# Performance work log

Measured on AMD Instinct MI355X. Metric: run time of the kernel, lower is better.

The kernel has to match this reference:

```python
import jax, jax.numpy as jnp
import numpy as np

B, H, W, C = 8, 32, 32, 384
NH, HD = 6, 64
SCALE = HD ** -0.5


def setup_inputs() -> dict:
    key = jax.random.key(0)
    ks = jax.random.split(key, 7)
    return {
        "x": jax.random.normal(ks[0], (B, H, W, C), jnp.float32),
        "qkv_w": jax.random.normal(ks[1], (C, 3 * C), jnp.float32) * 0.02,
        "qkv_b": jax.random.normal(ks[2], (3 * C,), jnp.float32) * 0.02,
        "proj_w": jax.random.normal(ks[3], (C, C), jnp.float32) * 0.02,
        "proj_b": jax.random.normal(ks[4], (C,), jnp.float32) * 0.02,
        "rel_pos_h": jax.random.normal(ks[5], (2 * H - 1, HD), jnp.float32) * 0.02,
        "rel_pos_w": jax.random.normal(ks[6], (2 * W - 1, HD), jnp.float32) * 0.02,
    }


def _get_rel_pos(rel_pos, q_size, k_size):
    # q_size == k_size and rel_pos already has 2*size-1 rows -> interpolation is identity
    coords = jnp.arange(q_size)[:, None] - jnp.arange(k_size)[None, :] + (k_size - 1)
    return rel_pos[coords]  # [q, k, head_dim]


def reference(x, qkv_w, qkv_b, proj_w, proj_b, rel_pos_h, rel_pos_w):
    b, h, w, c = x.shape
    hw = h * w
    qkv = x.reshape(b, hw, c) @ qkv_w + qkv_b            # [B, HW, 3C]
    qkv = qkv.reshape(b, hw, 3, NH, HD).transpose(2, 0, 3, 1, 4)
    qkv = qkv.reshape(3, b * NH, hw, HD)
    q, k, v = qkv[0], qkv[1], qkv[2]                      # [B*nH, HW, hd]

    attn = jnp.einsum('bqd,bkd->bqk', q * SCALE, k)       # [B*nH, HW, HW]

    Rh = _get_rel_pos(rel_pos_h, h, h)                    # [H, H, hd]
    Rw = _get_rel_pos(rel_pos_w, w, w)                    # [W, W, hd]
    r_q = q.reshape(b * NH, h, w, HD)
    rel_h = jnp.einsum('bhwc,hkc->bhwk', r_q, Rh)         # [B*nH, H, W, kH]
    rel_w = jnp.einsum('bhwc,wkc->bhwk', r_q, Rw)         # [B*nH, H, W, kW]
    attn = attn.reshape(b * NH, h, w, h, w) + rel_h[:, :, :, :, None] + rel_w[:, :, :, None, :]
    attn = attn.reshape(b * NH, hw, hw)

    attn = jax.nn.softmax(attn, axis=-1)
    out = jnp.einsum('bqk,bkd->bqd', attn, v)             # [B*nH, HW, hd]
    out = out.reshape(b, NH, h, w, HD).transpose(0, 2, 3, 1, 4).reshape(b, h, w, c)
    return out @ proj_w + proj_b
```

## Files before the change

kernel.cpp:

```cpp
#include <hip/hip_runtime.h>

typedef __attribute__((ext_vector_type(8))) short bf16x8;
typedef __attribute__((ext_vector_type(4))) float f32x4;

#define MFMA(a, b, c) __builtin_amdgcn_mfma_f32_16x16x32_bf16((a), (b), (c), 0, 0, 0)
#define LOG2E 1.4426950408889634f

__device__ __forceinline__ unsigned short f2bf(float f) {
    union { float f; unsigned u; } v; v.f = f;
    unsigned r = v.u + 0x7FFFu + ((v.u >> 16) & 1u);
    return (unsigned short)(r >> 16);
}
__device__ __forceinline__ float bf2f(unsigned short h) {
    union { unsigned u; float f; } v; v.u = ((unsigned)h) << 16;
    return v.f;
}
__device__ __forceinline__ float exp2fast(float x) {
#if __has_builtin(__builtin_amdgcn_exp2f)
    return __builtin_amdgcn_exp2f(x);
#else
    float r; asm("v_exp_f32 %0, %1" : "=v"(r) : "v"(x)); return r;
#endif
}
__device__ __forceinline__ void gload16(const void* g, void* l) {
    __builtin_amdgcn_global_load_lds(
        (const __attribute__((address_space(1))) void*)g,
        (__attribute__((address_space(3))) void*)l, 16, 0, 0);
}

#define WS_QHI   0
#define WS_QLO   6291456
#define WS_KHI   12582912
#define WS_KLO   18874368
#define WS_VTHI  25165824
#define WS_RELH  37748736
#define WS_RELW  40894464
#define WS_WTH   44040192
#define WS_WTL   44924928
#define WS_PWTH  45809664
#define WS_PWTL  46104576
#define WS_XHI   46399488
#define WS_XLO   52690944

__global__ __launch_bounds__(256) void prep_fused(const float* __restrict__ x,
        const float* __restrict__ qkv_w, const float* __restrict__ proj_w,
        unsigned short* __restrict__ xh,
        unsigned short* __restrict__ wth, unsigned short* __restrict__ pwth) {
    __shared__ float tile[64][65];
    const int bid = blockIdx.x;
    const int t = threadIdx.x;
    if (bid < 3072) {
        int i = bid * 256 + t;
        float4 v = ((const float4*)x)[i];
        float f[4] = {v.x, v.y, v.z, v.w};
#pragma unroll
        for (int j = 0; j < 4; ++j)
            xh[i * 4 + j] = f2bf(f[j]);
        return;
    }
    const float* w; unsigned short *oh; int K, N, bx, by;
    if (bid < 3180) {
        int b2 = bid - 3072;
        w = qkv_w; oh = wth; K = 384; N = 1152;
        bx = b2 % 18; by = b2 / 18;
    } else {
        int b3 = bid - 3180;
        w = proj_w; oh = pwth; K = 384; N = 384;
        bx = b3 % 6; by = b3 / 6;
    }
    const int k0 = by * 64, n0 = bx * 64;
#pragma unroll
    for (int i = 0; i < 16; ++i) {
        int idx = t + i * 256;
        int r = idx >> 6, c = idx & 63;
        tile[r][c] = w[(size_t)(k0 + r) * N + n0 + c];
    }
    __syncthreads();
#pragma unroll
    for (int i = 0; i < 16; ++i) {
        int idx = t + i * 256;
        int r = idx >> 6, c = idx & 63;
        oh[(size_t)(n0 + r) * K + k0 + c] = f2bf(tile[c][r]);
    }
}

__global__ __launch_bounds__(256) void qkv_gemm_mfma(
        const unsigned short* __restrict__ xh,
        const unsigned short* __restrict__ wth,
        const float* __restrict__ bias,
        unsigned short* __restrict__ qh,
        unsigned short* __restrict__ kh,
        unsigned short* __restrict__ vth) {
    __shared__ unsigned short Ah[2][4096], Bh[2][4096];
    const int t = threadIdx.x;
    const int lane = t & 63, wid = t >> 6;
    const int C = lane & 15, G = lane >> 4;
    const int nbid = (blockIdx.x & 7) * 288 + (blockIdx.x >> 3);
    const int row0 = (nbid / 18) * 64, col0 = (nbid % 18) * 64;
    const int rl = wid * 16 + (lane >> 3);
    const int cbyt = ((lane & 7) << 4) ^ ((lane >> 3) << 4);
    const char* pAh = (const char*)xh + (size_t)(row0 + rl) * 768 + cbyt;
    const char* pBh = (const char*)wth + (size_t)(col0 + rl) * 768 + cbyt;
    const int dof = wid * 2048;
    gload16(pAh, (char*)Ah[0] + dof); gload16(pAh + 6144, (char*)Ah[0] + dof + 1024);
    gload16(pBh, (char*)Bh[0] + dof); gload16(pBh + 6144, (char*)Bh[0] + dof + 1024);
    int cur = 0;
    f32x4 acc[4] = {};
    for (int kb = 0; kb < 6; ++kb) {
        if (kb < 5) {
            const int o = (kb + 1) * 128;
            gload16(pAh + o, (char*)Ah[cur^1] + dof); gload16(pAh + o + 6144, (char*)Ah[cur^1] + dof + 1024);
            gload16(pBh + o, (char*)Bh[cur^1] + dof); gload16(pBh + o + 6144, (char*)Bh[cur^1] + dof + 1024);
            __builtin_amdgcn_sched_barrier(0);
            asm volatile("s_waitcnt vmcnt(4)" ::: "memory");
        } else {
            asm volatile("s_waitcnt vmcnt(0)" ::: "memory");
        }
        __builtin_amdgcn_s_barrier();
        __builtin_amdgcn_sched_barrier(0);
        const unsigned short* AhB = Ah[cur];
        const unsigned short* BhB = Bh[cur];
#pragma unroll
        for (int ks = 0; ks < 2; ++ks) {
            int arow = wid * 16 + C;
            int aoff = arow * 128 + ((ks * 64 + G * 16) ^ ((arow & 7) << 4));
            bf16x8 ah = *(const bf16x8*)((char*)AhB + aoff);
#pragma unroll
            for (int s = 0; s < 4; ++s) {
                int brow = s * 16 + C;
                int boff = brow * 128 + ((ks * 64 + G * 16) ^ ((brow & 7) << 4));
                bf16x8 bh = *(const bf16x8*)((char*)BhB + boff);
                acc[s] = MFMA(ah, bh, acc[s]);
            }
        }
        __builtin_amdgcn_s_barrier();
        cur ^= 1;
    }
#pragma unroll
    for (int s = 0; s < 4; ++s) {
        int n = col0 + s * 16 + C;
        float bv = bias[n];
        int tsel = n / 384;
        int rem = n - tsel * 384;
        int head = rem >> 6, d = rem & 63;
#pragma unroll
        for (int r = 0; r < 4; ++r) {
            int m = row0 + wid * 16 + 4 * G + r;
            int b = m >> 10, hw = m & 1023;
            int g = b * 6 + head;
            float val = acc[s][r] + bv;
            if (tsel == 0) val *= 0.125f * LOG2E;
            unsigned short h = f2bf(val);
            if (tsel == 2) {
                vth[((size_t)g * 64 + d) * 1024 + hw] = h;
            } else {
                size_t o = ((size_t)g * 1024 + hw) * 64 + d;
                if (tsel == 0) qh[o] = h;
                else           kh[o] = h;
            }
        }
    }
}

__global__ __launch_bounds__(256) void rel_mfma(
        const unsigned short* __restrict__ qh,
        const float* __restrict__ rph, const float* __restrict__ rpw,
        unsigned short* __restrict__ relh, unsigned short* __restrict__ relw) {
    __shared__ unsigned short Bs[32 * 64];
    const int t = threadIdx.x;
    const int lane = t & 63, wid = t >> 6;
    const int C = lane & 15, G = lane >> 4;
    const int pos = blockIdx.x;
    const int g0 = blockIdx.y * 8;
    const int mode = blockIdx.z;
    const float* rp = (mode == 0) ? rph : rpw;
    {
        int k = t >> 3, d8 = t & 7;
        const float* src = rp + (size_t)(pos + 31 - k) * 64 + d8 * 8;
        float4 f0 = *(const float4*)src;
        float4 f1 = *(const float4*)(src + 4);
        unsigned short hv[8] = { f2bf(f0.x), f2bf(f0.y), f2bf(f0.z), f2bf(f0.w),
                                 f2bf(f1.x), f2bf(f1.y), f2bf(f1.z), f2bf(f1.w) };
        int bo = k * 128 + ((d8 * 16) ^ ((k & 7) << 4));
        *(bf16x8*)((char*)Bs + bo) = *(bf16x8*)hv;
    }
    __syncthreads();
    bf16x8 bf[2][2];
#pragma unroll
    for (int s = 0; s < 2; ++s)
#pragma unroll
        for (int ks = 0; ks < 2; ++ks) {
            int row = s * 16 + C;
            int off = row * 128 + ((ks * 64 + G * 16) ^ ((row & 7) << 4));
            bf[s][ks] = *(const bf16x8*)((char*)Bs + off);
        }
#pragma unroll
    for (int ib = 0; ib < 4; ++ib) {
        int arow = ib * 64 + wid * 16 + C;
        int gi = arow >> 5, w = arow & 31;
        int hw = (mode == 0) ? (pos * 32 + w) : (w * 32 + pos);
        const unsigned short* qrow = qh + ((size_t)(g0 + gi) * 1024 + hw) * 64;
        bf16x8 a0 = *(const bf16x8*)(qrow + G * 8);
        bf16x8 a1 = *(const bf16x8*)(qrow + 32 + G * 8);
        f32x4 acc[2] = {};
#pragma unroll
        for (int s = 0; s < 2; ++s) {
            acc[s] = MFMA(a0, bf[s][0], acc[s]);
            acc[s] = MFMA(a1, bf[s][1], acc[s]);
        }
        unsigned short* dst = (mode == 0) ? relh : relw;
#pragma unroll
        for (int s = 0; s < 2; ++s)
#pragma unroll
            for (int rr = 0; rr < 4; ++rr) {
                int orow = ib * 64 + wid * 16 + 4 * G + rr;
                int ogi = orow >> 5, ow = orow & 31;
                int ohw = (mode == 0) ? (pos * 32 + ow) : (ow * 32 + pos);
                dst[((size_t)(g0 + ogi) * 1024 + ohw) * 32 + s * 16 + C] =
                    f2bf(acc[s][rr] * 8.0f);
            }
    }
}

__global__ __launch_bounds__(256) void attn_mfma(
        const unsigned short* __restrict__ qh,
        const unsigned short* __restrict__ kh_g,
        const unsigned short* __restrict__ vth_g,
        const unsigned short* __restrict__ relh, const unsigned short* __restrict__ relw,
        unsigned short* __restrict__ atth) {
    __shared__ unsigned short Kh[2][4096], Vh[2][4096];
    __shared__ unsigned short Pl[4][1024];
    __shared__ unsigned short RelU[4][16 * 34];
    const int t = threadIdx.x;
    const int lane = t & 63, wid = t >> 6;
    const int C = lane & 15, G = lane >> 4;
    const int bid = blockIdx.x;
    const int wgid = (bid & 7) * 96 + (bid >> 3);
    const int g = wgid >> 4, qb = wgid & 15;
    const int qtile = qb * 64 + wid * 16;

    {
        const unsigned short* src = relh + ((size_t)g * 1024 + qb * 64) * 32;
#pragma unroll
        for (int j = 0; j < 8; ++j) {
            int i = t + j * 256;
            int row = i >> 5, col = i & 31;
            RelU[row >> 4][(row & 15) * 34 + col] = src[i];
        }
    }
    const int cbyt = ((lane & 7) << 4) ^ ((lane >> 3) << 4);
    const char* khbase = (const char*)(kh_g + (size_t)g * 65536)
                         + (wid * 16 + (lane >> 3)) * 128 + cbyt;
    const char* vhbase = (const char*)(vth_g + (size_t)g * 65536)
                         + (wid * 16 + (lane >> 3)) * 2048 + cbyt;
    bf16x8 qfh[2];
    {
        size_t qo = ((size_t)g * 1024 + qtile + C) * 64;
        qfh[0] = *(const bf16x8*)(qh + qo + G * 8);
        qfh[1] = *(const bf16x8*)(qh + qo + 32 + G * 8);
    }
    float rw8[2][4];
    {
        const unsigned short* rwp = relw + ((size_t)g * 1024 + qtile + C) * 32;
#pragma unroll
        for (int e = 0; e < 2; ++e)
#pragma unroll
            for (int r = 0; r < 4; ++r)
                rw8[e][r] = bf2f(rwp[e * 16 + 4 * G + r]);
    }
    f32x4 O[4] = {};
    float m_ = -1e30f, l_ = 0.f;
    unsigned short* Pw = Pl[wid];

    __syncthreads();
    {
        char* dK = (char*)Kh[0] + wid * 2048;
        char* dV = (char*)Vh[0] + wid * 2048;
        gload16(khbase, dK); gload16(khbase + 1024, dK + 1024);
        gload16(vhbase, dV); gload16(vhbase + 16384, dV + 1024);
    }
    int cur = 0;

    for (int kb = 0; kb < 16; ++kb) {
        if (kb < 15) {
            char* dK = (char*)Kh[cur ^ 1] + wid * 2048;
            char* dV = (char*)Vh[cur ^ 1] + wid * 2048;
            const char* sK = khbase + (kb + 1) * 8192;
            const char* sV = vhbase + (kb + 1) * 128;
            gload16(sK, dK); gload16(sK + 1024, dK + 1024);
            gload16(sV, dV); gload16(sV + 16384, dV + 1024);
            __builtin_amdgcn_sched_barrier(0);
            asm volatile("s_waitcnt vmcnt(4)" ::: "memory");
        } else {
            asm volatile("s_waitcnt vmcnt(0)" ::: "memory");
        }
        __builtin_amdgcn_s_barrier();
        __builtin_amdgcn_sched_barrier(0);
        const unsigned short* khbuf = Kh[cur];
        const unsigned short* vhbuf = Vh[cur];
        f32x4 S[4] = {};
        __builtin_amdgcn_s_setprio(1);
#pragma unroll
        for (int ks = 0; ks < 2; ++ks) {
#pragma unroll
            for (int s = 0; s < 4; ++s) {
                int row = s * 16 + C;
                int off = row * 128 + ((ks * 64 + G * 16) ^ ((row & 7) << 4));
                bf16x8 bh = *(const bf16x8*)((char*)khbuf + off);
                S[s] = MFMA(bh, qfh[ks], S[s]);
            }
        }
        __builtin_amdgcn_s_setprio(0);
        {
            unsigned rp = *(const unsigned*)((const char*)&RelU[wid][0]
                                             + C * 68 + 4 * kb);
            float rh0 = bf2f((unsigned short)(rp & 0xFFFF));
            float rh1 = bf2f((unsigned short)(rp >> 16));
#pragma unroll
            for (int s = 0; s < 4; ++s) {
                float rh = (s < 2) ? rh0 : rh1;
#pragma unroll
                for (int r = 0; r < 4; ++r)
                    S[s][r] += rh + rw8[s & 1][r];
            }
        }
        float mt = fmaxf(fmaxf(fmaxf(S[0][0], S[0][1]), fmaxf(S[0][2], S[0][3])),
                         fmaxf(fmaxf(S[1][0], S[1][1]), fmaxf(S[1][2], S[1][3])));
        mt = fmaxf(mt, fmaxf(fmaxf(fmaxf(S[2][0], S[2][1]), fmaxf(S[2][2], S[2][3])),
                             fmaxf(fmaxf(S[3][0], S[3][1]), fmaxf(S[3][2], S[3][3]))));
        mt = fmaxf(mt, __shfl_xor(mt, 16));
        mt = fmaxf(mt, __shfl_xor(mt, 32));
        if (__any(mt - m_ > 11.f)) {
            float mn = fmaxf(m_, mt);
            float corr = exp2fast(m_ - mn);
            m_ = mn;
            l_ *= corr;
            float cO[4];
#pragma unroll
            for (int r = 0; r < 4; ++r) cO[r] = __shfl(corr, 4 * G + r);
#pragma unroll
            for (int s = 0; s < 4; ++s)
#pragma unroll
                for (int r = 0; r < 4; ++r) O[s][r] *= cO[r];
        }
        float lt = 0.f;
#pragma unroll
        for (int s = 0; s < 4; ++s)
#pragma unroll
            for (int r = 0; r < 4; ++r) {
                S[s][r] = exp2fast(S[s][r] - m_);
                lt += S[s][r];
            }
        l_ += lt;
#pragma unroll
        for (int s = 0; s < 4; ++s) {
            unsigned d0, d1;
            asm("v_cvt_pk_bf16_f32 %0, %1, %2" : "=v"(d0) : "v"(S[s][0]), "v"(S[s][1]));
            asm("v_cvt_pk_bf16_f32 %0, %1, %2" : "=v"(d1) : "v"(S[s][2]), "v"(S[s][3]));
            int bo = C * 128 + (((s * 16 + 4 * G) * 2) ^ ((C & 7) << 4));
            uint2 dv; dv.x = d0; dv.y = d1;
            *(uint2*)((char*)Pw + bo) = dv;
        }
        __builtin_amdgcn_s_setprio(1);
#pragma unroll
        for (int ks = 0; ks < 2; ++ks) {
            int aoff = C * 128 + ((ks * 64 + G * 16) ^ ((C & 7) << 4));
            bf16x8 pa = *(const bf16x8*)((char*)Pw + aoff);
#pragma unroll
            for (int s = 0; s < 4; ++s) {
                int vrow = s * 16 + C;
                int voff = vrow * 128 + ((ks * 64 + G * 16) ^ ((vrow & 7) << 4));
                bf16x8 vh = *(const bf16x8*)((char*)vhbuf + voff);
                O[s] = MFMA(pa, vh, O[s]);
            }
        }
        __builtin_amdgcn_s_setprio(0);
        __builtin_amdgcn_s_barrier();
        cur ^= 1;
    }
    l_ += __shfl_xor(l_, 16);
    l_ += __shfl_xor(l_, 32);
    const int b = g / 6, head = g - b * 6;
#pragma unroll
    for (int r = 0; r < 4; ++r) {
        float inv = 1.0f / __shfl(l_, 4 * G + r);
        int token = qtile + 4 * G + r;
        size_t ob = ((size_t)b * 1024 + token) * 384 + head * 64;
#pragma unroll
        for (int s = 0; s < 4; ++s)
            atth[ob + s * 16 + C] = f2bf(O[s][r] * inv);
    }
}

__global__ __launch_bounds__(256) void proj_gemm_mfma(
        const unsigned short* __restrict__ ah_g,
        const unsigned short* __restrict__ bth,
        const float* __restrict__ bias, float* __restrict__ out) {
    __shared__ unsigned short Ah[2][4096], Bh[2][4096];
    const int t = threadIdx.x;
    const int lane = t & 63, wid = t >> 6;
    const int C = lane & 15, G = lane >> 4;
    const int nbid = (blockIdx.x & 7) * 96 + (blockIdx.x >> 3);
    const int row0 = (nbid / 6) * 64, col0 = (nbid % 6) * 64;
    const int rl = wid * 16 + (lane >> 3);
    const int cbyt = ((lane & 7) << 4) ^ ((lane >> 3) << 4);
    const char* pAh = (const char*)ah_g + (size_t)(row0 + rl) * 768 + cbyt;
    const char* pBh = (const char*)bth + (size_t)(col0 + rl) * 768 + cbyt;
    const int dof = wid * 2048;
    gload16(pAh, (char*)Ah[0] + dof); gload16(pAh + 6144, (char*)Ah[0] + dof + 1024);
    gload16(pBh, (char*)Bh[0] + dof); gload16(pBh + 6144, (char*)Bh[0] + dof + 1024);
    int cur = 0;
    f32x4 acc[4] = {};
    for (int kb = 0; kb < 6; ++kb) {
        if (kb < 5) {
            const int o = (kb + 1) * 128;
            gload16(pAh + o, (char*)Ah[cur^1] + dof); gload16(pAh + o + 6144, (char*)Ah[cur^1] + dof + 1024);
            gload16(pBh + o, (char*)Bh[cur^1] + dof); gload16(pBh + o + 6144, (char*)Bh[cur^1] + dof + 1024);
            __builtin_amdgcn_sched_barrier(0);
            asm volatile("s_waitcnt vmcnt(4)" ::: "memory");
        } else {
            asm volatile("s_waitcnt vmcnt(0)" ::: "memory");
        }
        __builtin_amdgcn_s_barrier();
        __builtin_amdgcn_sched_barrier(0);
        const unsigned short* AhB = Ah[cur];
        const unsigned short* BhB = Bh[cur];
#pragma unroll
        for (int ks = 0; ks < 2; ++ks) {
            int arow = wid * 16 + C;
            int aoff = arow * 128 + ((ks * 64 + G * 16) ^ ((arow & 7) << 4));
            bf16x8 ah = *(const bf16x8*)((char*)AhB + aoff);
#pragma unroll
            for (int s = 0; s < 4; ++s) {
                int brow = s * 16 + C;
                int boff = brow * 128 + ((ks * 64 + G * 16) ^ ((brow & 7) << 4));
                bf16x8 bh = *(const bf16x8*)((char*)BhB + boff);
                acc[s] = MFMA(ah, bh, acc[s]);
            }
        }
        __builtin_amdgcn_s_barrier();
        cur ^= 1;
    }
#pragma unroll
    for (int s = 0; s < 4; ++s) {
        int n = col0 + s * 16 + C;
        float bv = bias[n];
#pragma unroll
        for (int r = 0; r < 4; ++r) {
            int m = row0 + wid * 16 + 4 * G + r;
            out[(size_t)m * 384 + n] = acc[s][r] + bv;
        }
    }
}

extern "C" void kernel_launch(void* const* d_in, const int* in_sizes, int n_in,
                              void* d_out, int out_size, void* d_ws, size_t ws_size,
                              hipStream_t stream) {
    const float* x      = (const float*)d_in[0];
    const float* qkv_w  = (const float*)d_in[1];
    const float* qkv_b  = (const float*)d_in[2];
    const float* proj_w = (const float*)d_in[3];
    const float* proj_b = (const float*)d_in[4];
    const float* rph    = (const float*)d_in[5];
    const float* rpw    = (const float*)d_in[6];
    char* ws = (char*)d_ws;

    unsigned short* QHI  = (unsigned short*)(ws + WS_QHI);
    unsigned short* KHI  = (unsigned short*)(ws + WS_KHI);
    unsigned short* VTHI = (unsigned short*)(ws + WS_VTHI);
    unsigned short* RELH = (unsigned short*)(ws + WS_RELH);
    unsigned short* RELW = (unsigned short*)(ws + WS_RELW);
    unsigned short* WTH  = (unsigned short*)(ws + WS_WTH);
    unsigned short* PWTH = (unsigned short*)(ws + WS_PWTH);
    unsigned short* XHI  = (unsigned short*)(ws + WS_XHI);
    unsigned short* ATTH = XHI;

    prep_fused<<<3216, 256, 0, stream>>>(x, qkv_w, proj_w, XHI, WTH, PWTH);
    qkv_gemm_mfma<<<2304, 256, 0, stream>>>(XHI, WTH, qkv_b, QHI, KHI, VTHI);
    rel_mfma<<<dim3(32, 6, 2), 256, 0, stream>>>(QHI, rph, rpw, RELH, RELW);
    attn_mfma<<<768, 256, 0, stream>>>(QHI, KHI, VTHI, RELH, RELW, ATTH);
    proj_gemm_mfma<<<768, 256, 0, stream>>>(ATTH, PWTH, proj_b, (float*)d_out);
}
```

Baseline: 78.47 us.

## Enlarge QKV GEMM tile to 128 rows, vectorize bf16 stores, use fused max3

```diff
diff --git a/kernel.cpp b/kernel.cpp
--- a/kernel.cpp
+++ b/kernel.cpp
@@ -21,6 +21,9 @@
 #else
     float r; asm("v_exp_f32 %0, %1" : "=v"(r) : "v"(x)); return r;
 #endif
+}
+__device__ __forceinline__ float fm3(float a, float b, float c) {
+    return fmaxf(fmaxf(a, b), c);
 }
 __device__ __forceinline__ void gload16(const void* g, void* l) {
     __builtin_amdgcn_global_load_lds(
@@ -52,10 +55,10 @@
     if (bid < 3072) {
         int i = bid * 256 + t;
         float4 v = ((const float4*)x)[i];
-        float f[4] = {v.x, v.y, v.z, v.w};
-#pragma unroll
-        for (int j = 0; j < 4; ++j)
-            xh[i * 4 + j] = f2bf(f[j]);
+        uint2 o;
+        o.x = (unsigned)f2bf(v.x) | ((unsigned)f2bf(v.y) << 16);
+        o.y = (unsigned)f2bf(v.z) | ((unsigned)f2bf(v.w) << 16);
+        *(uint2*)&xh[i * 4] = o;
         return;
     }
     const float* w; unsigned short *oh; int K, N, bx, by;
@@ -91,28 +94,37 @@
         unsigned short* __restrict__ qh,
         unsigned short* __restrict__ kh,
         unsigned short* __restrict__ vth) {
-    __shared__ unsigned short Ah[2][4096], Bh[2][4096];
+    __shared__ unsigned short Ah[2][8192], Bh[2][4096];
     const int t = threadIdx.x;
     const int lane = t & 63, wid = t >> 6;
     const int C = lane & 15, G = lane >> 4;
-    const int nbid = (blockIdx.x & 7) * 288 + (blockIdx.x >> 3);
-    const int row0 = (nbid / 18) * 64, col0 = (nbid % 18) * 64;
-    const int rl = wid * 16 + (lane >> 3);
-    const int cbyt = ((lane & 7) << 4) ^ ((lane >> 3) << 4);
-    const char* pAh = (const char*)xh + (size_t)(row0 + rl) * 768 + cbyt;
-    const char* pBh = (const char*)wth + (size_t)(col0 + rl) * 768 + cbyt;
-    const int dof = wid * 2048;
-    gload16(pAh, (char*)Ah[0] + dof); gload16(pAh + 6144, (char*)Ah[0] + dof + 1024);
-    gload16(pBh, (char*)Bh[0] + dof); gload16(pBh + 6144, (char*)Bh[0] + dof + 1024);
+    const int nbid = (blockIdx.x & 7) * 144 + (blockIdx.x >> 3);
+    const int row0 = (nbid / 18) * 128, col0 = (nbid % 18) * 64;
+    const int rsub = lane >> 3;
+    const int cbyt = ((lane & 7) << 4) ^ (rsub << 4);
+    const char* pA = (const char*)xh + (size_t)(row0 + wid * 32 + rsub) * 768 + cbyt;
+    const char* pB = (const char*)wth + (size_t)(col0 + wid * 16 + rsub) * 768 + cbyt;
+    const int dofA = wid * 4096;
+    const int dofB = wid * 2048;
+    gload16(pA,         (char*)Ah[0] + dofA);
+    gload16(pA + 6144,  (char*)Ah[0] + dofA + 1024);
+    gload16(pA + 12288, (char*)Ah[0] + dofA + 2048);
+    gload16(pA + 18432, (char*)Ah[0] + dofA + 3072);
+    gload16(pB,         (char*)Bh[0] + dofB);
+    gload16(pB + 6144,  (char*)Bh[0] + dofB + 1024);
     int cur = 0;
-    f32x4 acc[4] = {};
+    f32x4 acc[2][4] = {};
     for (int kb = 0; kb < 6; ++kb) {
         if (kb < 5) {
             const int o = (kb + 1) * 128;
-            gload16(pAh + o, (char*)Ah[cur^1] + dof); gload16(pAh + o + 6144, (char*)Ah[cur^1] + dof + 1024);
-            gload16(pBh + o, (char*)Bh[cur^1] + dof); gload16(pBh + o + 6144, (char*)Bh[cur^1] + dof + 1024);
+            gload16(pA + o,         (char*)Ah[cur^1] + dofA);
+            gload16(pA + o + 6144,  (char*)Ah[cur^1] + dofA + 1024);
+            gload16(pA + o + 12288, (char*)Ah[cur^1] + dofA + 2048);
+            gload16(pA + o + 18432, (char*)Ah[cur^1] + dofA + 3072);
+            gload16(pB + o,         (char*)Bh[cur^1] + dofB);
+            gload16(pB + o + 6144,  (char*)Bh[cur^1] + dofB + 1024);
             __builtin_amdgcn_sched_barrier(0);
-            asm volatile("s_waitcnt vmcnt(4)" ::: "memory");
+            asm volatile("s_waitcnt vmcnt(6)" ::: "memory");
         } else {
             asm volatile("s_waitcnt vmcnt(0)" ::: "memory");
         }
@@ -122,16 +134,24 @@
         const unsigned short* BhB = Bh[cur];
 #pragma unroll
         for (int ks = 0; ks < 2; ++ks) {
-            int arow = wid * 16 + C;
-            int aoff = arow * 128 + ((ks * 64 + G * 16) ^ ((arow & 7) << 4));
-            bf16x8 ah = *(const bf16x8*)((char*)AhB + aoff);
+            bf16x8 ah[2], bh[4];
+#pragma unroll
+            for (int wr = 0; wr < 2; ++wr) {
+                int arow = wid * 32 + wr * 16 + C;
+                int aoff = arow * 128 + ((ks * 64 + G * 16) ^ ((arow & 7) << 4));
+                ah[wr] = *(const bf16x8*)((char*)AhB + aoff);
+            }
 #pragma unroll
             for (int s = 0; s < 4; ++s) {
                 int brow = s * 16 + C;
                 int boff = brow * 128 + ((ks * 64 + G * 16) ^ ((brow & 7) << 4));
-                bf16x8 bh = *(const bf16x8*)((char*)BhB + boff);
-                acc[s] = MFMA(ah, bh, acc[s]);
-            }
+                bh[s] = *(const bf16x8*)((char*)BhB + boff);
+            }
+#pragma unroll
+            for (int wr = 0; wr < 2; ++wr)
+#pragma unroll
+                for (int s = 0; s < 4; ++s)
+                    acc[wr][s] = MFMA(ah[wr], bh[s], acc[wr][s]);
         }
         __builtin_amdgcn_s_barrier();
         cur ^= 1;
@@ -144,21 +164,23 @@
         int rem = n - tsel * 384;
         int head = rem >> 6, d = rem & 63;
 #pragma unroll
-        for (int r = 0; r < 4; ++r) {
-            int m = row0 + wid * 16 + 4 * G + r;
-            int b = m >> 10, hw = m & 1023;
-            int g = b * 6 + head;
-            float val = acc[s][r] + bv;
-            if (tsel == 0) val *= 0.125f * LOG2E;
-            unsigned short h = f2bf(val);
-            if (tsel == 2) {
-                vth[((size_t)g * 64 + d) * 1024 + hw] = h;
-            } else {
-                size_t o = ((size_t)g * 1024 + hw) * 64 + d;
-                if (tsel == 0) qh[o] = h;
-                else           kh[o] = h;
-            }
-        }
+        for (int wr = 0; wr < 2; ++wr)
+#pragma unroll
+            for (int r = 0; r < 4; ++r) {
+                int m = row0 + wid * 32 + wr * 16 + 4 * G + r;
+                int b = m >> 10, hw = m & 1023;
+                int g = b * 6 + head;
+                float val = acc[wr][s][r] + bv;
+                if (tsel == 0) val *= 0.125f * LOG2E;
+                unsigned short h = f2bf(val);
+                if (tsel == 2) {
+                    vth[((size_t)g * 64 + d) * 1024 + hw] = h;
+                } else {
+                    size_t o = ((size_t)g * 1024 + hw) * 64 + d;
+                    if (tsel == 0) qh[o] = h;
+                    else           kh[o] = h;
+                }
+            }
     }
 }
 
@@ -324,10 +346,12 @@
                     S[s][r] += rh + rw8[s & 1][r];
             }
         }
-        float mt = fmaxf(fmaxf(fmaxf(S[0][0], S[0][1]), fmaxf(S[0][2], S[0][3])),
-                         fmaxf(fmaxf(S[1][0], S[1][1]), fmaxf(S[1][2], S[1][3])));
-        mt = fmaxf(mt, fmaxf(fmaxf(fmaxf(S[2][0], S[2][1]), fmaxf(S[2][2], S[2][3])),
-                             fmaxf(fmaxf(S[3][0], S[3][1]), fmaxf(S[3][2], S[3][3]))));
+        float mt = fm3(fm3(fm3(S[0][0], S[0][1], S[0][2]),
+                           fm3(S[0][3], S[1][0], S[1][1]),
+                           fm3(S[1][2], S[1][3], S[2][0])),
+                       fm3(S[2][1], S[2][2], S[2][3]),
+                       fm3(S[3][0], S[3][1], S[3][2]));
+        mt = fmaxf(mt, S[3][3]);
         mt = fmaxf(mt, __shfl_xor(mt, 16));
         mt = fmaxf(mt, __shfl_xor(mt, 32));
         if (__any(mt - m_ > 11.f)) {
@@ -476,7 +500,7 @@
     unsigned short* ATTH = XHI;
 
     prep_fused<<<3216, 256, 0, stream>>>(x, qkv_w, proj_w, XHI, WTH, PWTH);
-    qkv_gemm_mfma<<<2304, 256, 0, stream>>>(XHI, WTH, qkv_b, QHI, KHI, VTHI);
+    qkv_gemm_mfma<<<1152, 256, 0, stream>>>(XHI, WTH, qkv_b, QHI, KHI, VTHI);
     rel_mfma<<<dim3(32, 6, 2), 256, 0, stream>>>(QHI, rph, rpw, RELH, RELW);
     attn_mfma<<<768, 256, 0, stream>>>(QHI, KHI, VTHI, RELH, RELW, ATTH);
     proj_gemm_mfma<<<768, 256, 0, stream>>>(ATTH, PWTH, proj_b, (float*)d_out);
```

Measured after the change: 79.92 us. Within noise of the previous version (+1.8%).

## Widen attention blocks to 8 waves sharing K/V tiles; pack bf16 stores

Applied to the files above, without the earlier changes.

```diff
diff --git a/kernel.cpp b/kernel.cpp
--- a/kernel.cpp
+++ b/kernel.cpp
@@ -21,6 +21,9 @@
 #else
     float r; asm("v_exp_f32 %0, %1" : "=v"(r) : "v"(x)); return r;
 #endif
+}
+__device__ __forceinline__ float fm3(float a, float b, float c) {
+    return fmaxf(fmaxf(a, b), c);
 }
 __device__ __forceinline__ void gload16(const void* g, void* l) {
     __builtin_amdgcn_global_load_lds(
@@ -52,10 +55,10 @@
     if (bid < 3072) {
         int i = bid * 256 + t;
         float4 v = ((const float4*)x)[i];
-        float f[4] = {v.x, v.y, v.z, v.w};
-#pragma unroll
-        for (int j = 0; j < 4; ++j)
-            xh[i * 4 + j] = f2bf(f[j]);
+        uint2 o;
+        o.x = (unsigned)f2bf(v.x) | ((unsigned)f2bf(v.y) << 16);
+        o.y = (unsigned)f2bf(v.z) | ((unsigned)f2bf(v.w) << 16);
+        *(uint2*)&xh[i * 4] = o;
         return;
     }
     const float* w; unsigned short *oh; int K, N, bx, by;
@@ -222,37 +225,38 @@
     }
 }
 
-__global__ __launch_bounds__(256) void attn_mfma(
+__global__ __launch_bounds__(512) void attn_mfma(
         const unsigned short* __restrict__ qh,
         const unsigned short* __restrict__ kh_g,
         const unsigned short* __restrict__ vth_g,
         const unsigned short* __restrict__ relh, const unsigned short* __restrict__ relw,
         unsigned short* __restrict__ atth) {
     __shared__ unsigned short Kh[2][4096], Vh[2][4096];
-    __shared__ unsigned short Pl[4][1024];
-    __shared__ unsigned short RelU[4][16 * 34];
+    __shared__ unsigned short Pl[8][1024];
+    __shared__ unsigned short RelU[8][16 * 34];
     const int t = threadIdx.x;
     const int lane = t & 63, wid = t >> 6;
     const int C = lane & 15, G = lane >> 4;
     const int bid = blockIdx.x;
-    const int wgid = (bid & 7) * 96 + (bid >> 3);
-    const int g = wgid >> 4, qb = wgid & 15;
-    const int qtile = qb * 64 + wid * 16;
+    const int wgid = (bid & 7) * 48 + (bid >> 3);
+    const int g = wgid >> 3, qb = wgid & 7;
+    const int qtile = qb * 128 + wid * 16;
 
     {
-        const unsigned short* src = relh + ((size_t)g * 1024 + qb * 64) * 32;
+        const unsigned short* src = relh + ((size_t)g * 1024 + qb * 128) * 32;
 #pragma unroll
         for (int j = 0; j < 8; ++j) {
-            int i = t + j * 256;
+            int i = t + j * 512;
             int row = i >> 5, col = i & 31;
             RelU[row >> 4][(row & 15) * 34 + col] = src[i];
         }
     }
-    const int cbyt = ((lane & 7) << 4) ^ ((lane >> 3) << 4);
+    const int rsub = lane >> 3;
+    const int cbyt = ((lane & 7) << 4) ^ (rsub << 4);
     const char* khbase = (const char*)(kh_g + (size_t)g * 65536)
-                         + (wid * 16 + (lane >> 3)) * 128 + cbyt;
+                         + (wid * 8 + rsub) * 128 + cbyt;
     const char* vhbase = (const char*)(vth_g + (size_t)g * 65536)
-                         + (wid * 16 + (lane >> 3)) * 2048 + cbyt;
+                         + (wid * 8 + rsub) * 2048 + cbyt;
     bf16x8 qfh[2];
     {
         size_t qo = ((size_t)g * 1024 + qtile + C) * 64;
@@ -273,24 +277,16 @@
     unsigned short* Pw = Pl[wid];
 
     __syncthreads();
-    {
-        char* dK = (char*)Kh[0] + wid * 2048;
-        char* dV = (char*)Vh[0] + wid * 2048;
-        gload16(khbase, dK); gload16(khbase + 1024, dK + 1024);
-        gload16(vhbase, dV); gload16(vhbase + 16384, dV + 1024);
-    }
+    gload16(khbase, (char*)Kh[0] + wid * 1024);
+    gload16(vhbase, (char*)Vh[0] + wid * 1024);
     int cur = 0;
 
     for (int kb = 0; kb < 16; ++kb) {
         if (kb < 15) {
-            char* dK = (char*)Kh[cur ^ 1] + wid * 2048;
-            char* dV = (char*)Vh[cur ^ 1] + wid * 2048;
-            const char* sK = khbase + (kb + 1) * 8192;
-            const char* sV = vhbase + (kb + 1) * 128;
-            gload16(sK, dK); gload16(sK + 1024, dK + 1024);
-            gload16(sV, dV); gload16(sV + 16384, dV + 1024);
+            gload16(khbase + (kb + 1) * 8192, (char*)Kh[cur ^ 1] + wid * 1024);
+            gload16(vhbase + (kb + 1) * 128,  (char*)Vh[cur ^ 1] + wid * 1024);
             __builtin_amdgcn_sched_barrier(0);
-            asm volatile("s_waitcnt vmcnt(4)" ::: "memory");
+            asm volatile("s_waitcnt vmcnt(2)" ::: "memory");
         } else {
             asm volatile("s_waitcnt vmcnt(0)" ::: "memory");
         }
@@ -324,10 +320,12 @@
                     S[s][r] += rh + rw8[s & 1][r];
             }
         }
-        float mt = fmaxf(fmaxf(fmaxf(S[0][0], S[0][1]), fmaxf(S[0][2], S[0][3])),
-                         fmaxf(fmaxf(S[1][0], S[1][1]), fmaxf(S[1][2], S[1][3])));
-        mt = fmaxf(mt, fmaxf(fmaxf(fmaxf(S[2][0], S[2][1]), fmaxf(S[2][2], S[2][3])),
-                             fmaxf(fmaxf(S[3][0], S[3][1]), fmaxf(S[3][2], S[3][3]))));
+        float mt = fm3(fm3(fm3(S[0][0], S[0][1], S[0][2]),
+                           fm3(S[0][3], S[1][0], S[1][1]),
+                           fm3(S[1][2], S[1][3], S[2][0])),
+                       fm3(S[2][1], S[2][2], S[2][3]),
+                       fm3(S[3][0], S[3][1], S[3][2]));
+        mt = fmaxf(mt, S[3][3]);
         mt = fmaxf(mt, __shfl_xor(mt, 16));
         mt = fmaxf(mt, __shfl_xor(mt, 32));
         if (__any(mt - m_ > 11.f)) {
@@ -478,6 +476,6 @@
     prep_fused<<<3216, 256, 0, stream>>>(x, qkv_w, proj_w, XHI, WTH, PWTH);
     qkv_gemm_mfma<<<2304, 256, 0, stream>>>(XHI, WTH, qkv_b, QHI, KHI, VTHI);
     rel_mfma<<<dim3(32, 6, 2), 256, 0, stream>>>(QHI, rph, rpw, RELH, RELW);
-    attn_mfma<<<768, 256, 0, stream>>>(QHI, KHI, VTHI, RELH, RELW, ATTH);
+    attn_mfma<<<384, 512, 0, stream>>>(QHI, KHI, VTHI, RELH, RELW, ATTH);
     proj_gemm_mfma<<<768, 256, 0, stream>>>(ATTH, PWTH, proj_b, (float*)d_out);
 }
```

New measurement: 79.04 us. Within noise of the previous version (+0.7%).
